# Kernel tuning notes

Measured on AMD Instinct MI355X. Metric: run time of the kernel, lower is better.

Reference implementation:

```python
import jax, jax.numpy as jnp
import numpy as np

EPS = 1e-5


def setup_inputs() -> dict:
    key = jax.random.key(0)
    k_u, k_v, k_w, k_g, k_b, k_m, k_var = jax.random.split(key, 7)
    B, S, C1, C2, H, W = 4, 8, 64, 64, 128, 128
    CC = C1 + C2  # concat channels = out channels = 128
    u = jax.random.normal(k_u, (B, 1, C1, H, W), dtype=jnp.float32)
    v = jax.random.normal(k_v, (B, S, C2, H, W), dtype=jnp.float32)
    conv_w = jax.random.normal(k_w, (CC, CC, 3, 3), dtype=jnp.float32) * 0.05  # OIHW
    bn_gamma = jnp.ones((CC,), jnp.float32) + 0.1 * jax.random.normal(k_g, (CC,), dtype=jnp.float32)
    bn_beta = 0.1 * jax.random.normal(k_b, (CC,), dtype=jnp.float32)
    bn_mean = 0.1 * jax.random.normal(k_m, (CC,), dtype=jnp.float32)
    bn_var = jnp.abs(jax.random.normal(k_var, (CC,), dtype=jnp.float32)) + 0.5
    return {"u": u, "v": v, "conv_w": conv_w, "bn_gamma": bn_gamma,
            "bn_beta": bn_beta, "bn_mean": bn_mean, "bn_var": bn_var}


def _cross_conv(u, v, conv_w, bn_gamma, bn_beta, bn_mean, bn_var):
    B, _, C1, H, W = u.shape
    _, S, C2, _, _ = v.shape
    # broadcast u over the s axis, concat channels -> (b*s, c1+c2, h, w)
    us = jnp.broadcast_to(u[:, 0, None], (B, S, C1, H, W))
    xy = jnp.concatenate([us, v], axis=2).reshape(B * S, C1 + C2, H, W)
    # 3x3 conv, stride 1, SAME padding, no bias (BN follows)
    y = jax.lax.conv_general_dilated(
        xy, conv_w, window_strides=(1, 1), padding=((1, 1), (1, 1)),
        dimension_numbers=("NCHW", "OIHW", "NCHW"))
    # BatchNorm (inference: running stats)
    scale = (bn_gamma * jax.lax.rsqrt(bn_var + EPS))[None, :, None, None]
    shift = (bn_beta - bn_mean * bn_gamma * jax.lax.rsqrt(bn_var + EPS))[None, :, None, None]
    y = y * scale + shift
    # skip = Identity (concat_channels == out_channels, stride 1), then ReLU
    out = jax.nn.relu(y + xy)
    return out.reshape(B, 1, S, C1 + C2, H, W)


def reference(u, v, conv_w, bn_gamma, bn_beta, bn_mean, bn_var):
    return _cross_conv(u, v, conv_w, bn_gamma, bn_beta, bn_mean, bn_var)
```

## Files before the change

kernel.cpp:

```cpp
#include <hip/hip_runtime.h>
#include <hip/hip_bf16.h>


#define EPS 1e-5f

typedef __attribute__((ext_vector_type(8))) short short8;
typedef __attribute__((ext_vector_type(4))) float f32x4;
typedef __attribute__((ext_vector_type(2))) float f32x2;

constexpr int C1 = 64, CC = 128, Hd = 128, Wd = 128;
constexpr int HW = Hd * Wd;
constexpr int SP = 18;
constexpr int ROW = 40;
constexpr int WFRAGS = 9 * 4 * 8;
constexpr int NCHUNK = 18;
constexpr int UNITS = 16 * 18 * 10;
constexpr int NTHR = 512;
constexpr int NU = (UNITS + NTHR - 1) / NTHR;

__global__ void prep_weights(const float* __restrict__ wgt, ushort* __restrict__ wf) {
    int idx = blockIdx.x * 256 + threadIdx.x;
    if (idx >= WFRAGS * 64) return;
    int l  = idx & 63;
    int f  = idx >> 6;
    int cf = f & 7;
    int c  = (f >> 3) & 3;
    int t  = f >> 5;
    int kh = t / 3, kw = t % 3;
    int co  = cf * 16 + (l & 15);
    int cib = c * 32 + (l >> 4) * 8;
    ushort* dst = wf + (size_t)idx * 8;
#pragma unroll
    for (int j = 0; j < 8; ++j) {
        float x = wgt[(((size_t)co * CC + cib + j) * 3 + kh) * 3 + kw];
        __hip_bfloat16 bb = __float2bfloat16(x);
        dst[j] = *(ushort*)&bb;
    }
}

__global__ __launch_bounds__(NTHR, 2)
void crossconv_mfma(const float* __restrict__ u,
                    const float* __restrict__ v,
                    const ushort* __restrict__ wf,
                    const float* __restrict__ gamma,
                    const float* __restrict__ beta,
                    const float* __restrict__ mean,
                    const float* __restrict__ var,
                    float* __restrict__ out) {
    __shared__ alignas(16) ushort in_s[2][SP * SP * ROW];
    __shared__ float s_sc[CC], s_sh[CC];

    const int tid = threadIdx.x;
    const int w0 = blockIdx.x * 16;
    const int h0 = blockIdx.y * 16;
    const int b  = blockIdx.z;
    const float* __restrict__ ubase = u + (size_t)b * C1 * HW;
    const float* __restrict__ vbase = v + (size_t)b * 8 * C1 * HW;

    if (tid < CC) {
        float sc = gamma[tid] * rsqrtf(var[tid] + EPS);
        s_sc[tid] = sc;
        s_sh[tid] = beta[tid] - mean[tid] * sc;
    }
    {
        uint4 z{0u, 0u, 0u, 0u};
        uint4* p = (uint4*)&in_s[0][0];
        for (int i = tid; i < 2 * SP * SP * ROW / 8; i += NTHR) p[i] = z;
    }

    const int l = tid & 63, wid = tid >> 6;
    const int n16 = l & 15, kgrp = l >> 4;

    f32x4 accU[8][2], accV[8][2];
#pragma unroll
    for (int cf = 0; cf < 8; ++cf) {
        accU[cf][0] = (f32x4)0.f; accU[cf][1] = (f32x4)0.f;
    }

    f32x2 sa[NU], sb[NU];
    int   sidx[NU];
    uint  sm0 = 0, sm1 = 0;

    auto chunk_src = [&](int k) -> const float* {
        if (k < 2) return ubase + (size_t)k * 32 * HW;
        int km = k - 2;
        return vbase + ((size_t)(km >> 1) * C1 + (size_t)(km & 1) * 32) * HW;
    };

    auto stage_load = [&](const float* __restrict__ src) {
        sm0 = sm1 = 0;
#pragma unroll
        for (int i = 0; i < NU; ++i) {
            int e = tid + i * NTHR;
            sa[i] = f32x2{0.f, 0.f}; sb[i] = f32x2{0.f, 0.f}; sidx[i] = 0;
            if (e < UNITS) {
                int cp  = e / 180;
                int r   = e - cp * 180;
                int sph = r / 10;
                int j   = r - sph * 10;
                int gh  = h0 + sph - 1;
                int gw  = w0 + 2 * j - 2;
                sidx[i] = (sph * SP + 2 * j) * ROW + 2 * cp;
                if ((unsigned)gh < (unsigned)Hd && (unsigned)gw < (unsigned)(Wd - 1)) {
                    const float* p = src + (size_t)(2 * cp) * HW + gh * Wd + gw;
                    sa[i] = *(const f32x2*)p;
                    sb[i] = *(const f32x2*)(p + HW);
                    if (j >= 1) sm0 |= 1u << i;
                    if (j <= 8) sm1 |= 1u << i;
                }
            }
        }
    };

    auto stage_write = [&](int buf) {
        ushort* __restrict__ d = in_s[buf];
#pragma unroll
        for (int i = 0; i < NU; ++i) {
            __hip_bfloat16 ax = __float2bfloat16(sa[i].x);
            __hip_bfloat16 bx = __float2bfloat16(sb[i].x);
            __hip_bfloat16 ay = __float2bfloat16(sa[i].y);
            __hip_bfloat16 by = __float2bfloat16(sb[i].y);
            uint v0 = (uint)*(ushort*)&ax | ((uint)*(ushort*)&bx << 16);
            uint v1 = (uint)*(ushort*)&ay | ((uint)*(ushort*)&by << 16);
            if (sm0 & (1u << i)) *(uint*)&d[sidx[i] - ROW] = v0;
            if (sm1 & (1u << i)) *(uint*)&d[sidx[i]]       = v1;
        }
    };

    auto compute = [&](int buf, int c, f32x4 (&acc)[8][2]) {
        const ushort* __restrict__ bs = in_s[buf];
#pragma unroll
        for (int t = 0; t < 9; ++t) {
            const int kh = t / 3, kw = t % 3;
            const int spw = n16 + kw;
            short8 p0 = *(const short8*)&bs[((wid * 2 + 0 + kh) * SP + spw) * ROW + kgrp * 8];
            short8 p1 = *(const short8*)&bs[((wid * 2 + 1 + kh) * SP + spw) * ROW + kgrp * 8];
            const short8* __restrict__ wp =
                (const short8*)wf + ((size_t)(t * 4 + c) * 8) * 64 + l;
#pragma unroll
            for (int cf = 0; cf < 8; ++cf) {
                short8 wfr = wp[(size_t)cf * 64];
                acc[cf][0] = __builtin_amdgcn_mfma_f32_16x16x32_bf16(p0, wfr, acc[cf][0], 0, 0, 0);
                acc[cf][1] = __builtin_amdgcn_mfma_f32_16x16x32_bf16(p1, wfr, acc[cf][1], 0, 0, 0);
            }
        }
    };

    __syncthreads();
    stage_load(chunk_src(0));
    stage_write(0);
    __syncthreads();

    for (int k = 0; k < NCHUNK; ++k) {
        const int cur = k & 1;
        if (k + 1 < NCHUNK) stage_load(chunk_src(k + 1));
        if (k >= 2 && (k & 1) == 0) {
#pragma unroll
            for (int cf = 0; cf < 8; ++cf) {
                accV[cf][0] = accU[cf][0]; accV[cf][1] = accU[cf][1];
            }
        }
        const int c = (k < 2) ? k : 2 + ((k - 2) & 1);
        if (k < 2) compute(cur, c, accU);
        else       compute(cur, c, accV);
        if (k + 1 < NCHUNK) stage_write(cur ^ 1);
        if (k >= 3 && (k & 1)) {
            const int s = (k - 3) >> 1;
            const size_t n = (size_t)b * 8 + s;
#pragma unroll
            for (int cf = 0; cf < 8; ++cf) {
                const int co = cf * 16 + n16;
                const float sc = s_sc[co], sh = s_sh[co];
                const float* __restrict__ xb = (cf < 4)
                    ? (ubase + (size_t)co * HW)
                    : (vbase + ((size_t)s * C1 + (co - C1)) * HW);
                float* __restrict__ ob = out + ((size_t)n * CC + co) * HW;
#pragma unroll
                for (int pf = 0; pf < 2; ++pf) {
                    const int off = (h0 + wid * 2 + pf) * Wd + w0 + kgrp * 4;
                    f32x4 x = *(const f32x4*)(xb + off);
                    f32x4 a = accV[cf][pf];
                    f32x4 y;
#pragma unroll
                    for (int r = 0; r < 4; ++r)
                        y[r] = fmaxf(fmaf(a[r], sc, sh) + x[r], 0.f);
                    *(f32x4*)(ob + off) = y;
                }
            }
        }
        __syncthreads();
    }
}

extern "C" void kernel_launch(void* const* d_in, const int* in_sizes, int n_in,
                              void* d_out, int out_size, void* d_ws, size_t ws_size,
                              hipStream_t stream) {
    const float* u     = (const float*)d_in[0];
    const float* v     = (const float*)d_in[1];
    const float* wgt   = (const float*)d_in[2];
    const float* gamma = (const float*)d_in[3];
    const float* beta  = (const float*)d_in[4];
    const float* mean  = (const float*)d_in[5];
    const float* var   = (const float*)d_in[6];
    float* out = (float*)d_out;
    ushort* wf = (ushort*)d_ws;

    prep_weights<<<dim3((WFRAGS * 64 + 255) / 256), dim3(256), 0, stream>>>(wgt, wf);
    crossconv_mfma<<<dim3(Wd / 16, Hd / 16, 4), dim3(NTHR), 0, stream>>>(
        u, v, wf, gamma, beta, mean, var, out);
}
```

Baseline: 977.4 us.

## Split grid per (batch, s) and recompute u-channel conv contribution per block

Launches one block per (batch, sequence) tile instead of per batch, so each block processes only 4 channel chunks and writes a single output. The shared u-channel partial convolution is no longer reused across s and is recomputed in every block, roughly doubling MMA work. Staging offsets and masks are also precomputed once outside the chunk loop. The intent is to fill the GPU with many more blocks and shorten each block's serial chain.

```diff
diff --git a/kernel.cpp b/kernel.cpp
--- a/kernel.cpp
+++ b/kernel.cpp
@@ -13,9 +13,8 @@
 constexpr int SP = 18;
 constexpr int ROW = 40;
 constexpr int WFRAGS = 9 * 4 * 8;
-constexpr int NCHUNK = 18;
+constexpr int NTHR = 512;
 constexpr int UNITS = 16 * 18 * 10;
-constexpr int NTHR = 512;
 constexpr int NU = (UNITS + NTHR - 1) / NTHR;
 
 __global__ void prep_weights(const float* __restrict__ wgt, ushort* __restrict__ wf) {
@@ -53,9 +52,10 @@
     const int tid = threadIdx.x;
     const int w0 = blockIdx.x * 16;
     const int h0 = blockIdx.y * 16;
-    const int b  = blockIdx.z;
+    const int n  = blockIdx.z;
+    const int b  = n >> 3;
     const float* __restrict__ ubase = u + (size_t)b * C1 * HW;
-    const float* __restrict__ vbase = v + (size_t)b * 8 * C1 * HW;
+    const float* __restrict__ vbase = v + (size_t)n * C1 * HW;
 
     if (tid < CC) {
         float sc = gamma[tid] * rsqrtf(var[tid] + EPS);
@@ -65,53 +65,57 @@
     {
         uint4 z{0u, 0u, 0u, 0u};
         uint4* p = (uint4*)&in_s[0][0];
-        for (int i = tid; i < 2 * SP * SP * ROW / 8; i += NTHR) p[i] = z;
+        for (int i = tid; i < 2 * SP * SP * ROW * 2 / 16; i += NTHR) p[i] = z;
     }
 
     const int l = tid & 63, wid = tid >> 6;
     const int n16 = l & 15, kgrp = l >> 4;
 
-    f32x4 accU[8][2], accV[8][2];
-#pragma unroll
-    for (int cf = 0; cf < 8; ++cf) {
-        accU[cf][0] = (f32x4)0.f; accU[cf][1] = (f32x4)0.f;
-    }
+    int  goff[NU];
+    int  sidx[NU];
+    uint lm = 0, m0 = 0, m1 = 0;
+#pragma unroll
+    for (int i = 0; i < NU; ++i) {
+        goff[i] = 0; sidx[i] = ROW;
+        int e = tid + i * NTHR;
+        if (e < UNITS) {
+            int cp  = e / 180;
+            int r   = e - cp * 180;
+            int sph = r / 10;
+            int j   = r - sph * 10;
+            int gh  = h0 + sph - 1;
+            int gw  = w0 + 2 * j - 2;
+            sidx[i] = (sph * SP + 2 * j) * ROW + 2 * cp;
+            if ((unsigned)gh < (unsigned)Hd && (unsigned)gw < (unsigned)(Wd - 1)) {
+                goff[i] = 2 * cp * HW + gh * Wd + gw;
+                lm |= 1u << i;
+                if (j >= 1) m0 |= 1u << i;
+                if (j <= 8) m1 |= 1u << i;
+            }
+        }
+    }
+
+    f32x4 acc[8][2];
+#pragma unroll
+    for (int cf = 0; cf < 8; ++cf) { acc[cf][0] = (f32x4)0.f; acc[cf][1] = (f32x4)0.f; }
 
     f32x2 sa[NU], sb[NU];
-    int   sidx[NU];
-    uint  sm0 = 0, sm1 = 0;
-
-    auto chunk_src = [&](int k) -> const float* {
-        if (k < 2) return ubase + (size_t)k * 32 * HW;
-        int km = k - 2;
-        return vbase + ((size_t)(km >> 1) * C1 + (size_t)(km & 1) * 32) * HW;
-    };
-
+
+    auto chunk_src = [&](int c) -> const float* {
+        return (c < 2) ? ubase + (size_t)c * 32 * HW
+                       : vbase + (size_t)(c - 2) * 32 * HW;
+    };
     auto stage_load = [&](const float* __restrict__ src) {
-        sm0 = sm1 = 0;
 #pragma unroll
         for (int i = 0; i < NU; ++i) {
-            int e = tid + i * NTHR;
-            sa[i] = f32x2{0.f, 0.f}; sb[i] = f32x2{0.f, 0.f}; sidx[i] = 0;
-            if (e < UNITS) {
-                int cp  = e / 180;
-                int r   = e - cp * 180;
-                int sph = r / 10;
-                int j   = r - sph * 10;
-                int gh  = h0 + sph - 1;
-                int gw  = w0 + 2 * j - 2;
-                sidx[i] = (sph * SP + 2 * j) * ROW + 2 * cp;
-                if ((unsigned)gh < (unsigned)Hd && (unsigned)gw < (unsigned)(Wd - 1)) {
-                    const float* p = src + (size_t)(2 * cp) * HW + gh * Wd + gw;
-                    sa[i] = *(const f32x2*)p;
-                    sb[i] = *(const f32x2*)(p + HW);
-                    if (j >= 1) sm0 |= 1u << i;
-                    if (j <= 8) sm1 |= 1u << i;
-                }
+            sa[i] = f32x2{0.f, 0.f}; sb[i] = f32x2{0.f, 0.f};
+            if (lm & (1u << i)) {
+                const float* p = src + goff[i];
+                sa[i] = *(const f32x2*)p;
+                sb[i] = *(const f32x2*)(p + HW);
             }
         }
     };
-
     auto stage_write = [&](int buf) {
         ushort* __restrict__ d = in_s[buf];
 #pragma unroll
@@ -122,12 +126,11 @@
             __hip_bfloat16 by = __float2bfloat16(sb[i].y);
             uint v0 = (uint)*(ushort*)&ax | ((uint)*(ushort*)&bx << 16);
             uint v1 = (uint)*(ushort*)&ay | ((uint)*(ushort*)&by << 16);
-            if (sm0 & (1u << i)) *(uint*)&d[sidx[i] - ROW] = v0;
-            if (sm1 & (1u << i)) *(uint*)&d[sidx[i]]       = v1;
-        }
-    };
-
-    auto compute = [&](int buf, int c, f32x4 (&acc)[8][2]) {
+            if (m0 & (1u << i)) *(uint*)&d[sidx[i] - ROW] = v0;
+            if (m1 & (1u << i)) *(uint*)&d[sidx[i]]       = v1;
+        }
+    };
+    auto compute = [&](int buf, int c) {
         const ushort* __restrict__ bs = in_s[buf];
 #pragma unroll
         for (int t = 0; t < 9; ++t) {
@@ -146,49 +149,36 @@
         }
     };
 
+    stage_load(chunk_src(0));
     __syncthreads();
-    stage_load(chunk_src(0));
     stage_write(0);
     __syncthreads();
 
-    for (int k = 0; k < NCHUNK; ++k) {
-        const int cur = k & 1;
-        if (k + 1 < NCHUNK) stage_load(chunk_src(k + 1));
-        if (k >= 2 && (k & 1) == 0) {
-#pragma unroll
-            for (int cf = 0; cf < 8; ++cf) {
-                accV[cf][0] = accU[cf][0]; accV[cf][1] = accU[cf][1];
-            }
-        }
-        const int c = (k < 2) ? k : 2 + ((k - 2) & 1);
-        if (k < 2) compute(cur, c, accU);
-        else       compute(cur, c, accV);
-        if (k + 1 < NCHUNK) stage_write(cur ^ 1);
-        if (k >= 3 && (k & 1)) {
-            const int s = (k - 3) >> 1;
-            const size_t n = (size_t)b * 8 + s;
-#pragma unroll
-            for (int cf = 0; cf < 8; ++cf) {
-                const int co = cf * 16 + n16;
-                const float sc = s_sc[co], sh = s_sh[co];
-                const float* __restrict__ xb = (cf < 4)
-                    ? (ubase + (size_t)co * HW)
-                    : (vbase + ((size_t)s * C1 + (co - C1)) * HW);
-                float* __restrict__ ob = out + ((size_t)n * CC + co) * HW;
-#pragma unroll
-                for (int pf = 0; pf < 2; ++pf) {
-                    const int off = (h0 + wid * 2 + pf) * Wd + w0 + kgrp * 4;
-                    f32x4 x = *(const f32x4*)(xb + off);
-                    f32x4 a = accV[cf][pf];
-                    f32x4 y;
-#pragma unroll
-                    for (int r = 0; r < 4; ++r)
-                        y[r] = fmaxf(fmaf(a[r], sc, sh) + x[r], 0.f);
-                    *(f32x4*)(ob + off) = y;
-                }
-            }
-        }
+    for (int c = 0; c < 4; ++c) {
+        if (c < 3) stage_load(chunk_src(c + 1));
+        compute(c & 1, c);
+        if (c < 3) stage_write((c & 1) ^ 1);
         __syncthreads();
+    }
+
+#pragma unroll
+    for (int cf = 0; cf < 8; ++cf) {
+        const int co = cf * 16 + n16;
+        const float sc = s_sc[co], sh = s_sh[co];
+        const float* __restrict__ xb = (cf < 4) ? (ubase + (size_t)co * HW)
+                                                : (vbase + (size_t)(co - C1) * HW);
+        float* __restrict__ ob = out + ((size_t)n * CC + co) * HW;
+#pragma unroll
+        for (int pf = 0; pf < 2; ++pf) {
+            const int off = (h0 + wid * 2 + pf) * Wd + w0 + kgrp * 4;
+            f32x4 x = *(const f32x4*)(xb + off);
+            f32x4 a = acc[cf][pf];
+            f32x4 y;
+#pragma unroll
+            for (int r = 0; r < 4; ++r)
+                y[r] = fmaxf(fmaf(a[r], sc, sh) + x[r], 0.f);
+            *(f32x4*)(ob + off) = y;
+        }
     }
 }
 
@@ -206,6 +196,6 @@
     ushort* wf = (ushort*)d_ws;
 
     prep_weights<<<dim3((WFRAGS * 64 + 255) / 256), dim3(256), 0, stream>>>(wgt, wf);
-    crossconv_mfma<<<dim3(Wd / 16, Hd / 16, 4), dim3(NTHR), 0, stream>>>(
+    crossconv_mfma<<<dim3(Wd / 16, Hd / 16, 32), dim3(NTHR), 0, stream>>>(
         u, v, wf, gamma, beta, mean, var, out);
 }
```

New measurement: 1.007 ms. 3.0% more time.
